# Performance work log

Measured on AMD Instinct MI355X. Metric: run time of the kernel, lower is better.

## Reference

```python
import jax, jax.numpy as jnp
import numpy as np

E = 8192   # line-graph nodes (edges of g)
N = 4096   # graph nodes
FIN = 64   # in_feats
FOUT = 64  # out_feats
H = FOUT // 2
BN_EPS = 1e-5


def _linear_params(k, fan_in):
    kw, kb = jax.random.split(k)
    s = 1.0 / np.sqrt(fan_in)
    w = jax.random.uniform(kw, (H, fan_in), jnp.float32, -s, s)
    b = jax.random.uniform(kb, (H,), jnp.float32, -s, s)
    return w, b


def setup_inputs() -> dict:
    key = jax.random.key(0)
    ks = jax.random.split(key, 12)
    inp = {}
    inp["y"] = jax.random.normal(ks[0], (E, FIN), jnp.float32)
    inp["deg_g"] = jax.random.uniform(ks[1], (N,), jnp.float32)  # unused in forward
    inp["g_a1"] = jnp.zeros((N, N), jnp.float32)                  # unused in forward
    # adjacency-like 0/1 matrices, sparse pattern stored dense (as th.mm expects)
    inp["lg_a1"] = (jax.random.uniform(ks[2], (E, E)) < (8.0 / E)).astype(jnp.float32)
    inp["pm"] = (jax.random.uniform(ks[3], (N, E)) < (2.0 / N)).astype(jnp.float32)
    inp["pd"] = (jax.random.uniform(ks[4], (N, E)) < (2.0 / N)).astype(jnp.float32)
    inp["theta_y_w"], inp["theta_y_b"] = _linear_params(ks[5], FIN)
    inp["theta_y_r_w"], inp["theta_y_r_b"] = _linear_params(ks[6], FIN)
    inp["gamma_a_w"], inp["gamma_a_b"] = _linear_params(ks[7], FIN)
    inp["gamma_x_w"], inp["gamma_x_b"] = _linear_params(ks[8], FOUT)
    inp["gamma_a_r_w"], inp["gamma_a_r_b"] = _linear_params(ks[9], FIN)
    inp["gamma_x_r_w"], inp["gamma_x_r_b"] = _linear_params(ks[10], FOUT)
    inp["bn_x_w"] = jnp.ones((FOUT,), jnp.float32)
    inp["bn_x_b"] = jnp.zeros((FOUT,), jnp.float32)
    inp["bn_y_w"] = jnp.ones((FOUT,), jnp.float32)
    inp["bn_y_b"] = jnp.zeros((FOUT,), jnp.float32)
    return inp


def _bn(x, w, b):
    # BatchNorm2d on [B, C, 1, 1] in training mode == per-channel batch norm
    # with biased variance over the row (batch) dimension.
    m = x.mean(0)
    v = jnp.mean((x - m) ** 2, axis=0)
    return (x - m) * jax.lax.rsqrt(v + BN_EPS) * w + b


def reference(y, deg_g, g_a1, lg_a1, pm, pd,
              theta_y_w, theta_y_b, theta_y_r_w, theta_y_r_b,
              gamma_a_w, gamma_a_b, gamma_x_w, gamma_x_b,
              gamma_a_r_w, gamma_a_r_b, gamma_x_r_w, gamma_x_r_b,
              bn_x_w, bn_x_b, bn_y_w, bn_y_b):
    pd_y = pd @ y                                        # [N, FIN]
    x_r = pd_y @ theta_y_r_w.T + theta_y_r_b             # [N, H]
    x = pd_y @ theta_y_w.T + theta_y_b                   # [N, H]
    x = jnp.concatenate([x, jax.nn.relu(x_r)], axis=1)   # [N, FOUT]
    x = _bn(x, bn_x_w, bn_x_b)
    pm_x = pm.T @ x                                      # [E, FOUT]
    lg_y = lg_a1 @ y                                     # [E, FIN] (computed once; torch computes it twice, same math)
    y_r = (lg_y @ gamma_a_r_w.T + gamma_a_r_b) + (pm_x @ gamma_x_r_w.T + gamma_x_r_b)
    y_n = (lg_y @ gamma_a_w.T + gamma_a_b) + (pm_x @ gamma_x_w.T + gamma_x_b)
    y_out = jnp.concatenate([y_n, jax.nn.relu(y_r)], axis=1)  # [E, FOUT]
    return _bn(y_out, bn_y_w, bn_y_b)
```

## Files before the change

kernel.cpp:

```cpp
#include <hip/hip_runtime.h>

typedef unsigned int uint_t;
typedef unsigned short ushort_t;
typedef unsigned long long ull_t;
typedef uint_t nvec4 __attribute__((ext_vector_type(4)));

#define SLOTS 48

__device__ __forceinline__ float bcast(float v, int k) {
    union { float f; int i; } x; x.f = v;
    int r = __builtin_amdgcn_readlane(x.i, k);
    union { int i; float f; } y2; y2.i = r;
    return y2.f;
}

__global__ __launch_bounds__(256) void stream_gather_kernel(
    const float* __restrict__ lg, const float* __restrict__ pd,
    const float* __restrict__ pm, const float* __restrict__ y,
    float* __restrict__ lg_y, float* __restrict__ pd_y,
    ushort_t* __restrict__ pm_keys, uint_t* __restrict__ pm_counts)
{
    __shared__ ushort_t sIdx[4][SLOTS];
    const int lane = threadIdx.x & 63;
    const int wv = threadIdx.x >> 6;
    const int wid = blockIdx.x * 4 + wv;
    const float* A;
    int row;
    if (wid < 8192)       { row = wid;         A = lg; }
    else if (wid < 12288) { row = wid - 8192;  A = pd; }
    else                  { row = wid - 12288; A = pm; }

    const nvec4* ap = (const nvec4*)(A + (size_t)row * 8192);
    ushort_t* slice = sIdx[wv];
    const ull_t lt = (1ull << lane) - 1ull;

    nvec4 buf[16];
    #pragma unroll
    for (int i = 0; i < 16; ++i)
        buf[i] = __builtin_nontemporal_load(ap + i * 64 + lane);

    uint_t cnt = 0;
    #pragma unroll
    for (int pp = 0; pp < 32; pp += 16) {
        #pragma unroll
        for (int i = 0; i < 16; ++i) {
            nvec4 c = buf[i];
            if (pp == 0)
                buf[i] = __builtin_nontemporal_load(ap + (16 + i) * 64 + lane);
            uint_t a0 = c.x, a1 = c.y, a2 = c.z, a3 = c.w;
            ull_t m = __ballot((a0 | a1 | a2 | a3) != 0u);
            if (m) {
                ull_t m0 = __ballot(a0 != 0u);
                ull_t m1 = __ballot(a1 != 0u);
                ull_t m2 = __ballot(a2 != 0u);
                ull_t m3 = __ballot(a3 != 0u);
                uint_t c0 = (uint_t)__popcll(m0), c1 = (uint_t)__popcll(m1);
                uint_t c2 = (uint_t)__popcll(m2);
                uint_t o0 = cnt + (uint_t)__popcll(m0 & lt);
                uint_t o1 = cnt + c0 + (uint_t)__popcll(m1 & lt);
                uint_t o2 = cnt + c0 + c1 + (uint_t)__popcll(m2 & lt);
                uint_t o3 = cnt + c0 + c1 + c2 + (uint_t)__popcll(m3 & lt);
                int j = (pp + i) * 256 + lane * 4;
                if (a0 && o0 < SLOTS) slice[o0] = (ushort_t)(j + 0);
                if (a1 && o1 < SLOTS) slice[o1] = (ushort_t)(j + 1);
                if (a2 && o2 < SLOTS) slice[o2] = (ushort_t)(j + 2);
                if (a3 && o3 < SLOTS) slice[o3] = (ushort_t)(j + 3);
                cnt += (uint_t)(__popcll(m0) + __popcll(m1) +
                                __popcll(m2) + __popcll(m3));
            }
        }
    }
    if (cnt > SLOTS) cnt = SLOTS;

    if (wid >= 12288) {
        if (lane == 0) pm_counts[row] = cnt;
        if (lane < (int)cnt) pm_keys[(size_t)row * SLOTS + lane] = slice[lane];
        return;
    }
    float a0 = 0.f, a1 = 0.f, a2 = 0.f, a3 = 0.f;
    uint_t i = 0;
    for (; i + 4 <= cnt; i += 4) {
        int j0 = slice[i + 0], j1 = slice[i + 1];
        int j2 = slice[i + 2], j3 = slice[i + 3];
        a0 += y[(size_t)j0 * 64 + lane];
        a1 += y[(size_t)j1 * 64 + lane];
        a2 += y[(size_t)j2 * 64 + lane];
        a3 += y[(size_t)j3 * 64 + lane];
    }
    for (; i < cnt; ++i) a0 += y[(size_t)slice[i] * 64 + lane];
    float acc = (a0 + a1) + (a2 + a3);
    if (wid < 8192) lg_y[(size_t)row * 64 + lane] = acc;
    else            pd_y[(size_t)row * 64 + lane] = acc;
}

__global__ __launch_bounds__(256) void xlin_kernel(
    const float* __restrict__ pd_y,
    const float* __restrict__ wt, const float* __restrict__ bt,
    const float* __restrict__ wr, const float* __restrict__ br,
    float* __restrict__ x_raw, float* __restrict__ stats_x)
{
    __shared__ float red[2][4][64];
    const int wave = threadIdx.x >> 6, lane = threadIdx.x & 63;
    const float* wsrc = (lane < 32) ? (wt + lane * 64) : (wr + (lane - 32) * 64);
    float wreg[64];
    const float4* wp = (const float4*)wsrc;
    #pragma unroll
    for (int q = 0; q < 16; ++q) {
        float4 t = wp[q];
        wreg[q * 4 + 0] = t.x; wreg[q * 4 + 1] = t.y;
        wreg[q * 4 + 2] = t.z; wreg[q * 4 + 3] = t.w;
    }
    float bias = (lane < 32) ? bt[lane] : br[lane - 32];
    float s1 = 0.f, s2 = 0.f;
    const int row0 = (blockIdx.x * 4 + wave) * 8;
    for (int r = 0; r < 8; ++r) {
        int row = row0 + r;
        float xv = pd_y[(size_t)row * 64 + lane];
        float acc = bias;
        #pragma unroll
        for (int k = 0; k < 64; ++k) acc = fmaf(bcast(xv, k), wreg[k], acc);
        if (lane >= 32) acc = fmaxf(acc, 0.f);
        x_raw[(size_t)row * 64 + lane] = acc;
        s1 += acc; s2 += acc * acc;
    }
    red[0][wave][lane] = s1; red[1][wave][lane] = s2;
    __syncthreads();
    if (wave == 0) {
        float a = 0.f, b = 0.f;
        #pragma unroll
        for (int w = 0; w < 4; ++w) { a += red[0][w][lane]; b += red[1][w][lane]; }
        atomicAdd(&stats_x[lane], a);
        atomicAdd(&stats_x[64 + lane], b);
    }
}

__global__ __launch_bounds__(256) void scatter_kernel(
    const ushort_t* __restrict__ pm_keys, const uint_t* __restrict__ pm_counts,
    const float* __restrict__ x_raw, const float* __restrict__ stats_x,
    const float* __restrict__ bnxw, const float* __restrict__ bnxb,
    float* __restrict__ pm_x)
{
    const int lane = threadIdx.x & 63;
    const int row = blockIdx.x * 4 + (threadIdx.x >> 6);
    float mean = stats_x[lane] * (1.f / 4096.f);
    float var  = fmaxf(stats_x[64 + lane] * (1.f / 4096.f) - mean * mean, 0.f);
    float rstd = rsqrtf(var + 1e-5f);
    float scale = rstd * bnxw[lane];
    float shift = bnxb[lane] - mean * scale;
    const ushort_t* slice = pm_keys + (size_t)row * SLOTS;
    uint_t cnt = pm_counts[row];
    float xb = fmaf(x_raw[(size_t)row * 64 + lane], scale, shift);
    for (uint_t i = 0; i < cnt; ++i) {
        int e = slice[i];
        atomicAdd(&pm_x[(size_t)e * 64 + lane], xb);
    }
}

__global__ __launch_bounds__(256) void ylin_kernel(
    const float* __restrict__ lg_y, const float* __restrict__ pm_x,
    const float* __restrict__ wa, const float* __restrict__ ba,
    const float* __restrict__ wx, const float* __restrict__ bx,
    const float* __restrict__ war, const float* __restrict__ bar,
    const float* __restrict__ wxr, const float* __restrict__ bxr,
    float* __restrict__ yraw, float* __restrict__ stats_y)
{
    __shared__ float red[2][4][64];
    const int wave = threadIdx.x >> 6, lane = threadIdx.x & 63;
    const float* s1p = (lane < 32) ? (wa + lane * 64) : (war + (lane - 32) * 64);
    const float* s2p = (lane < 32) ? (wx + lane * 64) : (wxr + (lane - 32) * 64);
    float w1[64], w2[64];
    {
        const float4* p1 = (const float4*)s1p;
        const float4* p2 = (const float4*)s2p;
        #pragma unroll
        for (int q = 0; q < 16; ++q) {
            float4 t1 = p1[q], t2 = p2[q];
            w1[q * 4 + 0] = t1.x; w1[q * 4 + 1] = t1.y;
            w1[q * 4 + 2] = t1.z; w1[q * 4 + 3] = t1.w;
            w2[q * 4 + 0] = t2.x; w2[q * 4 + 1] = t2.y;
            w2[q * 4 + 2] = t2.z; w2[q * 4 + 3] = t2.w;
        }
    }
    float bias = (lane < 32) ? (ba[lane] + bx[lane])
                             : (bar[lane - 32] + bxr[lane - 32]);
    float s1 = 0.f, s2 = 0.f;
    const int row0 = (blockIdx.x * 4 + wave) * 8;
    for (int r = 0; r < 8; ++r) {
        int row = row0 + r;
        float lv = lg_y[(size_t)row * 64 + lane];
        float pv = pm_x[(size_t)row * 64 + lane];
        float acc = bias;
        #pragma unroll
        for (int k = 0; k < 64; ++k) {
            acc = fmaf(bcast(lv, k), w1[k], acc);
            acc = fmaf(bcast(pv, k), w2[k], acc);
        }
        if (lane >= 32) acc = fmaxf(acc, 0.f);
        yraw[(size_t)row * 64 + lane] = acc;
        s1 += acc; s2 += acc * acc;
    }
    red[0][wave][lane] = s1; red[1][wave][lane] = s2;
    __syncthreads();
    if (wave == 0) {
        float a = 0.f, b = 0.f;
        #pragma unroll
        for (int w = 0; w < 4; ++w) { a += red[0][w][lane]; b += red[1][w][lane]; }
        atomicAdd(&stats_y[lane], a);
        atomicAdd(&stats_y[64 + lane], b);
    }
}

__global__ __launch_bounds__(256) void bny_kernel(
    float* __restrict__ yraw, const float* __restrict__ stats_y,
    const float* __restrict__ bnyw, const float* __restrict__ bnyb)
{
    int idx = blockIdx.x * 256 + threadIdx.x;
    int c = idx & 63;
    float mean = stats_y[c] * (1.f / 8192.f);
    float var  = fmaxf(stats_y[64 + c] * (1.f / 8192.f) - mean * mean, 0.f);
    float rstd = rsqrtf(var + 1e-5f);
    yraw[idx] = (yraw[idx] - mean) * rstd * bnyw[c] + bnyb[c];
}

extern "C" void kernel_launch(void* const* d_in, const int* in_sizes, int n_in,
                              void* d_out, int out_size, void* d_ws, size_t ws_size,
                              hipStream_t stream)
{
    const float* y     = (const float*)d_in[0];
    const float* lg_a1 = (const float*)d_in[3];
    const float* pm    = (const float*)d_in[4];
    const float* pd    = (const float*)d_in[5];
    const float* th_w  = (const float*)d_in[6];
    const float* th_b  = (const float*)d_in[7];
    const float* thr_w = (const float*)d_in[8];
    const float* thr_b = (const float*)d_in[9];
    const float* ga_w  = (const float*)d_in[10];
    const float* ga_b  = (const float*)d_in[11];
    const float* gx_w  = (const float*)d_in[12];
    const float* gx_b  = (const float*)d_in[13];
    const float* gar_w = (const float*)d_in[14];
    const float* gar_b = (const float*)d_in[15];
    const float* gxr_w = (const float*)d_in[16];
    const float* gxr_b = (const float*)d_in[17];
    const float* bnx_w = (const float*)d_in[18];
    const float* bnx_b = (const float*)d_in[19];
    const float* bny_w = (const float*)d_in[20];
    const float* bny_b = (const float*)d_in[21];

    char* ws = (char*)d_ws;
    float* stats_x = (float*)ws;
    float* stats_y = (float*)(ws + 1024);
    float* pm_x    = (float*)(ws + 2048);
    const size_t zero_bytes = 2048 + (size_t)8192 * 64 * 4;
    float* pd_y  = (float*)(ws + zero_bytes);
    float* lg_y  = pd_y + (size_t)4096 * 64;
    float* x_raw = lg_y + (size_t)8192 * 64;
    ushort_t* pm_keys = (ushort_t*)(x_raw + (size_t)4096 * 64);
    uint_t* pm_counts = (uint_t*)(pm_keys + (size_t)4096 * SLOTS);
    float* yraw  = (float*)d_out;

    (void)hipMemsetAsync(d_ws, 0, zero_bytes, stream);

    stream_gather_kernel<<<4096, 256, 0, stream>>>(lg_a1, pd, pm, y,
                                                   lg_y, pd_y,
                                                   pm_keys, pm_counts);
    xlin_kernel<<<128, 256, 0, stream>>>(pd_y, th_w, th_b, thr_w, thr_b,
                                         x_raw, stats_x);
    scatter_kernel<<<1024, 256, 0, stream>>>(pm_keys, pm_counts, x_raw, stats_x,
                                             bnx_w, bnx_b, pm_x);
    ylin_kernel<<<256, 256, 0, stream>>>(lg_y, pm_x, ga_w, ga_b, gx_w, gx_b,
                                         gar_w, gar_b, gxr_w, gxr_b,
                                         yraw, stats_y);
    bny_kernel<<<2048, 256, 0, stream>>>(yraw, stats_y, bny_w, bny_b);
}
```

Measured before the change: 574.5 us.

## Fuse x linear with pm scatter, defer BN-x affine into ylin via degree

Merges the x linear kernel and the scatter kernel. Raw, un-normalized x values are scattered into pm_x right away, and a per-edge degree count is accumulated alongside them. The BN-x scale and shift are applied later in ylin as scale*pm_x + shift*deg, which is algebraically equivalent. This removes one kernel launch and the x_raw round trip through memory, at the cost of extra atomics for the degree counts and a larger zeroed workspace.

```diff
diff --git a/kernel.cpp b/kernel.cpp
--- a/kernel.cpp
+++ b/kernel.cpp
@@ -93,34 +93,42 @@
     else            pd_y[(size_t)row * 64 + lane] = acc;
 }
 
-__global__ __launch_bounds__(256) void xlin_kernel(
+__global__ __launch_bounds__(256) void xscat_kernel(
     const float* __restrict__ pd_y,
+    const ushort_t* __restrict__ pm_keys, const uint_t* __restrict__ pm_counts,
     const float* __restrict__ wt, const float* __restrict__ bt,
     const float* __restrict__ wr, const float* __restrict__ br,
-    float* __restrict__ x_raw, float* __restrict__ stats_x)
+    float* __restrict__ pm_x, float* __restrict__ deg,
+    float* __restrict__ stats_x)
 {
     __shared__ float red[2][4][64];
     const int wave = threadIdx.x >> 6, lane = threadIdx.x & 63;
-    const float* wsrc = (lane < 32) ? (wt + lane * 64) : (wr + (lane - 32) * 64);
+    const int gwave = blockIdx.x * 4 + wave;
+
     float wreg[64];
-    const float4* wp = (const float4*)wsrc;
-    #pragma unroll
-    for (int q = 0; q < 16; ++q) {
-        float4 t = wp[q];
-        wreg[q * 4 + 0] = t.x; wreg[q * 4 + 1] = t.y;
-        wreg[q * 4 + 2] = t.z; wreg[q * 4 + 3] = t.w;
-    }
-    float bias = (lane < 32) ? bt[lane] : br[lane - 32];
+    {
+        const float* wsrc = (lane < 32) ? (wt + lane * 64)
+                                        : (wr + (lane - 32) * 64);
+        const float4* wp = (const float4*)wsrc;
+        #pragma unroll
+        for (int q = 0; q < 16; ++q) {
+            float4 t = wp[q];
+            wreg[q * 4 + 0] = t.x; wreg[q * 4 + 1] = t.y;
+            wreg[q * 4 + 2] = t.z; wreg[q * 4 + 3] = t.w;
+        }
+    }
+    float biasx = (lane < 32) ? bt[lane] : br[lane - 32];
+    float xr[4];
     float s1 = 0.f, s2 = 0.f;
-    const int row0 = (blockIdx.x * 4 + wave) * 8;
-    for (int r = 0; r < 8; ++r) {
-        int row = row0 + r;
-        float xv = pd_y[(size_t)row * 64 + lane];
-        float acc = bias;
+    const int xrow0 = gwave * 4;
+    #pragma unroll
+    for (int r = 0; r < 4; ++r) {
+        float xv = pd_y[(size_t)(xrow0 + r) * 64 + lane];
+        float acc = biasx;
         #pragma unroll
         for (int k = 0; k < 64; ++k) acc = fmaf(bcast(xv, k), wreg[k], acc);
         if (lane >= 32) acc = fmaxf(acc, 0.f);
-        x_raw[(size_t)row * 64 + lane] = acc;
+        xr[r] = acc;
         s1 += acc; s2 += acc * acc;
     }
     red[0][wave][lane] = s1; red[1][wave][lane] = s2;
@@ -132,32 +140,24 @@
         atomicAdd(&stats_x[lane], a);
         atomicAdd(&stats_x[64 + lane], b);
     }
-}
-
-__global__ __launch_bounds__(256) void scatter_kernel(
-    const ushort_t* __restrict__ pm_keys, const uint_t* __restrict__ pm_counts,
-    const float* __restrict__ x_raw, const float* __restrict__ stats_x,
-    const float* __restrict__ bnxw, const float* __restrict__ bnxb,
-    float* __restrict__ pm_x)
-{
-    const int lane = threadIdx.x & 63;
-    const int row = blockIdx.x * 4 + (threadIdx.x >> 6);
-    float mean = stats_x[lane] * (1.f / 4096.f);
-    float var  = fmaxf(stats_x[64 + lane] * (1.f / 4096.f) - mean * mean, 0.f);
-    float rstd = rsqrtf(var + 1e-5f);
-    float scale = rstd * bnxw[lane];
-    float shift = bnxb[lane] - mean * scale;
-    const ushort_t* slice = pm_keys + (size_t)row * SLOTS;
-    uint_t cnt = pm_counts[row];
-    float xb = fmaf(x_raw[(size_t)row * 64 + lane], scale, shift);
-    for (uint_t i = 0; i < cnt; ++i) {
-        int e = slice[i];
-        atomicAdd(&pm_x[(size_t)e * 64 + lane], xb);
+
+    #pragma unroll
+    for (int r = 0; r < 4; ++r) {
+        int row = xrow0 + r;
+        uint_t cnt = pm_counts[row];
+        const ushort_t* slice = pm_keys + (size_t)row * SLOTS;
+        for (uint_t i = 0; i < cnt; ++i) {
+            int e = slice[i];
+            atomicAdd(&pm_x[(size_t)e * 64 + lane], xr[r]);
+            if (lane == 0) atomicAdd(&deg[e], 1.0f);
+        }
     }
 }
 
 __global__ __launch_bounds__(256) void ylin_kernel(
     const float* __restrict__ lg_y, const float* __restrict__ pm_x,
+    const float* __restrict__ deg, const float* __restrict__ stats_x,
+    const float* __restrict__ bnxw, const float* __restrict__ bnxb,
     const float* __restrict__ wa, const float* __restrict__ ba,
     const float* __restrict__ wx, const float* __restrict__ bx,
     const float* __restrict__ war, const float* __restrict__ bar,
@@ -181,6 +181,16 @@
             w2[q * 4 + 2] = t2.z; w2[q * 4 + 3] = t2.w;
         }
     }
+    float scx, shx;
+    {
+        float s = stats_x[lane];
+        float q = stats_x[64 + lane];
+        float mean = s * (1.f / 4096.f);
+        float var  = fmaxf(q * (1.f / 4096.f) - mean * mean, 0.f);
+        float rstd = rsqrtf(var + 1e-5f);
+        scx = rstd * bnxw[lane];
+        shx = bnxb[lane] - mean * scx;
+    }
     float bias = (lane < 32) ? (ba[lane] + bx[lane])
                              : (bar[lane - 32] + bxr[lane - 32]);
     float s1 = 0.f, s2 = 0.f;
@@ -188,7 +198,8 @@
     for (int r = 0; r < 8; ++r) {
         int row = row0 + r;
         float lv = lg_y[(size_t)row * 64 + lane];
-        float pv = pm_x[(size_t)row * 64 + lane];
+        float dg = deg[row];
+        float pv = fmaf(pm_x[(size_t)row * 64 + lane], scx, shx * dg);
         float acc = bias;
         #pragma unroll
         for (int k = 0; k < 64; ++k) {
@@ -250,12 +261,12 @@
     char* ws = (char*)d_ws;
     float* stats_x = (float*)ws;
     float* stats_y = (float*)(ws + 1024);
-    float* pm_x    = (float*)(ws + 2048);
-    const size_t zero_bytes = 2048 + (size_t)8192 * 64 * 4;
+    float* deg     = (float*)(ws + 2048);
+    float* pm_x    = (float*)(ws + 2048 + 32768);
+    const size_t zero_bytes = 2048 + 32768 + (size_t)8192 * 64 * 4;
     float* pd_y  = (float*)(ws + zero_bytes);
     float* lg_y  = pd_y + (size_t)4096 * 64;
-    float* x_raw = lg_y + (size_t)8192 * 64;
-    ushort_t* pm_keys = (ushort_t*)(x_raw + (size_t)4096 * 64);
+    ushort_t* pm_keys = (ushort_t*)(lg_y + (size_t)8192 * 64);
     uint_t* pm_counts = (uint_t*)(pm_keys + (size_t)4096 * SLOTS);
     float* yraw  = (float*)d_out;
 
@@ -264,11 +275,12 @@
     stream_gather_kernel<<<4096, 256, 0, stream>>>(lg_a1, pd, pm, y,
                                                    lg_y, pd_y,
                                                    pm_keys, pm_counts);
-    xlin_kernel<<<128, 256, 0, stream>>>(pd_y, th_w, th_b, thr_w, thr_b,
-                                         x_raw, stats_x);
-    scatter_kernel<<<1024, 256, 0, stream>>>(pm_keys, pm_counts, x_raw, stats_x,
-                                             bnx_w, bnx_b, pm_x);
-    ylin_kernel<<<256, 256, 0, stream>>>(lg_y, pm_x, ga_w, ga_b, gx_w, gx_b,
+    xscat_kernel<<<256, 256, 0, stream>>>(pd_y, pm_keys, pm_counts,
+                                          th_w, th_b, thr_w, thr_b,
+                                          pm_x, deg, stats_x);
+    ylin_kernel<<<256, 256, 0, stream>>>(lg_y, pm_x, deg, stats_x,
+                                         bnx_w, bnx_b,
+                                         ga_w, ga_b, gx_w, gx_b,
                                          gar_w, gar_b, gxr_w, gxr_b,
                                          yraw, stats_y);
     bny_kernel<<<2048, 256, 0, stream>>>(yraw, stats_y, bny_w, bny_b);
```

Measured after the change: 578.4 us. About the same (+0.7%).
